# Performance work log

Hardware: AMD Instinct MI355X
Metric: run time of the kernel (lower is better)

## Reference

```python
import jax, jax.numpy as jnp
import numpy as np

NUM_HEAD = 16


def setup_inputs() -> dict:
    key = jax.random.key(0)
    ks = jax.random.split(key, 7)
    B, S, E = 2, 2048, 1024
    scale = 0.02
    return {
        "x": jax.random.normal(ks[0], (B, S, E), dtype=jnp.float32),
        "Wq": jax.random.normal(ks[1], (E, E), dtype=jnp.float32) * scale,
        "bq": jax.random.normal(ks[2], (E,), dtype=jnp.float32) * scale,
        "Wk": jax.random.normal(ks[3], (E, E), dtype=jnp.float32) * scale,
        "bk": jax.random.normal(ks[4], (E,), dtype=jnp.float32) * scale,
        "Wv": jax.random.normal(ks[5], (E, E), dtype=jnp.float32) * scale,
        "bv": jax.random.normal(ks[6], (E,), dtype=jnp.float32) * scale,
    }


def reference(x, Wq, bq, Wk, bk, Wv, bv):
    B, S, E = x.shape
    H = NUM_HEAD
    Dh = E // H
    # torch Linear: y = x @ W.T + b
    q = (x @ Wq.T + bq).reshape(B, S, H, Dh).transpose(0, 2, 1, 3)  # [B,H,S,Dh]
    k = (x @ Wk.T + bk).reshape(B, S, H, Dh).transpose(0, 2, 1, 3)
    v = (x @ Wv.T + bv).reshape(B, S, H, Dh).transpose(0, 2, 1, 3)
    attn = jnp.einsum("bhqd,bhkd->bhqk", q, k) / jnp.sqrt(jnp.float32(Dh))
    score = jax.nn.softmax(attn, axis=-1)
    out = jnp.einsum("bhqk,bhkd->bhqd", score, v)  # [B,H,S,Dh]
    return out.transpose(0, 2, 1, 3).reshape(B, S, E)
```

## Files before the change

### kernel.cpp

```cpp
#include <hip/hip_runtime.h>
#include <hip/hip_bf16.h>
#include <stdint.h>

#define S_LEN 2048
#define E_DIM 1024
#define NHEAD 16
#define DHEAD 64
#define BATCH 2

typedef short bf16x8 __attribute__((ext_vector_type(8)));
typedef float f32x4 __attribute__((ext_vector_type(4)));
typedef float f32x16 __attribute__((ext_vector_type(16)));

__device__ __forceinline__ ushort f2bf(float f) {
    uint32_t u = __builtin_bit_cast(uint32_t, f);
    u += 0x7fffu + ((u >> 16) & 1u);
    return (ushort)(u >> 16);
}
__device__ __forceinline__ uint32_t cvtpk(float lo, float hi) {
    uint32_t r;
    asm("v_cvt_pk_bf16_f32 %0, %1, %2" : "=v"(r) : "v"(lo), "v"(hi));
    return r;
}
__device__ __forceinline__ f32x16 zero16() {
    f32x16 v;
    #pragma unroll
    for (int i = 0; i < 16; ++i) v[i] = 0.f;
    return v;
}
__device__ __forceinline__ void gload16(const void* g, void* l) {
    __builtin_amdgcn_global_load_lds(
        (const __attribute__((address_space(1))) uint32_t*)g,
        (__attribute__((address_space(3))) uint32_t*)l, 16, 0, 0);
}

__global__ __launch_bounds__(256) void convert_kernel(
    const float* __restrict__ x, const float* __restrict__ wq,
    const float* __restrict__ wk, const float* __restrict__ wv,
    ushort* __restrict__ xb, ushort* __restrict__ wqb,
    ushort* __restrict__ wkb, ushort* __restrict__ wvb)
{
    const int a = blockIdx.y;
    const float* src = (a == 0) ? x : (a == 1) ? wq : (a == 2) ? wk : wv;
    ushort* dst      = (a == 0) ? xb : (a == 1) ? wqb : (a == 2) ? wkb : wvb;
    const int n4 = (a == 0) ? (BATCH * S_LEN * E_DIM / 4) : (E_DIM * E_DIM / 4);
    const int idx = blockIdx.x * 256 + threadIdx.x;
    if (idx < n4) {
        float4 v = reinterpret_cast<const float4*>(src)[idx];
        ushort4 o;
        o.x = f2bf(v.x); o.y = f2bf(v.y); o.z = f2bf(v.z); o.w = f2bf(v.w);
        reinterpret_cast<ushort4*>(dst)[idx] = o;
    }
}

__global__ __launch_bounds__(256) void qkv_mfma_kernel(
    const ushort* __restrict__ xb, const ushort* __restrict__ wqb,
    const ushort* __restrict__ wkb, const ushort* __restrict__ wvb,
    const float* __restrict__ bq, const float* __restrict__ bk,
    const float* __restrict__ bv,
    ushort* __restrict__ qb, ushort* __restrict__ kb, ushort* __restrict__ vtb)
{
    const int z = blockIdx.z;
    const ushort* Ag; const ushort* Bg; const float* bias;
    int m0, n0;
    if (z == 2) { Ag = wvb; Bg = xb;                 bias = bv;
                  m0 = blockIdx.y * 128; n0 = blockIdx.x * 128; }
    else        { Ag = xb;  Bg = (z == 0) ? wqb : wkb; bias = (z == 0) ? bq : bk;
                  m0 = blockIdx.x * 128; n0 = blockIdx.y * 128; }

    __shared__ ushort As[128 * 64];
    __shared__ ushort Bs[128 * 64];

    const int tid  = threadIdx.x;
    const int lane = tid & 63;
    const int wid  = tid >> 6;
    const int wr   = wid >> 1, wc = wid & 1;

    f32x4 acc[4][4];
    #pragma unroll
    for (int i = 0; i < 4; ++i)
        #pragma unroll
        for (int j = 0; j < 4; ++j) acc[i][j] = (f32x4){0.f, 0.f, 0.f, 0.f};

    const int crow  = lane >> 3;
    const int cslot = lane & 7;
    const int lr    = lane & 15;
    const int lq    = lane >> 4;

    for (int k0 = 0; k0 < E_DIM; k0 += 64) {
        #pragma unroll
        for (int j = 0; j < 4; ++j) {
            const int rbase = wid * 32 + j * 8;
            const int srow  = rbase + crow;
            const int sslot = cslot ^ (srow & 7);
            gload16(&Ag[(size_t)(m0 + srow) * E_DIM + k0 + sslot * 8],
                    &As[rbase * 64]);
            gload16(&Bg[(size_t)(n0 + srow) * E_DIM + k0 + sslot * 8],
                    &Bs[rbase * 64]);
        }
        __syncthreads();

        #pragma unroll
        for (int ks = 0; ks < 2; ++ks) {
            bf16x8 af[4], bf[4];
            #pragma unroll
            for (int mi = 0; mi < 4; ++mi) {
                const int row  = wr * 64 + mi * 16 + lr;
                const int slot = (ks * 4 + lq) ^ (row & 7);
                af[mi] = *reinterpret_cast<const bf16x8*>(
                    &As[row * 64 + slot * 8]);
            }
            #pragma unroll
            for (int ni = 0; ni < 4; ++ni) {
                const int row  = wc * 64 + ni * 16 + lr;
                const int slot = (ks * 4 + lq) ^ (row & 7);
                bf[ni] = *reinterpret_cast<const bf16x8*>(
                    &Bs[row * 64 + slot * 8]);
            }
            #pragma unroll
            for (int mi = 0; mi < 4; ++mi)
                #pragma unroll
                for (int ni = 0; ni < 4; ++ni)
                    acc[mi][ni] = __builtin_amdgcn_mfma_f32_16x16x32_bf16(
                        af[mi], bf[ni], acc[mi][ni], 0, 0, 0);
        }
        __syncthreads();
    }

    const int rq = lane >> 4;
    #pragma unroll
    for (int mi = 0; mi < 4; ++mi) {
        #pragma unroll
        for (int ni = 0; ni < 4; ++ni) {
            #pragma unroll
            for (int r = 0; r < 4; ++r) {
                const int i = m0 + wr * 64 + mi * 16 + rq * 4 + r;
                const int j = n0 + wc * 64 + ni * 16 + lr;
                float val = acc[mi][ni][r];
                if (z == 2) {
                    val += bias[i];
                    const int h = i >> 6, d = i & 63;
                    const int b = j >> 11, s = j & (S_LEN - 1);
                    vtb[(((size_t)(b * NHEAD + h)) * DHEAD + d) * S_LEN + s] = f2bf(val);
                } else {
                    val += bias[j];
                    const int h = j >> 6, d = j & 63;
                    const int b = i >> 11, s = i & (S_LEN - 1);
                    ushort* o = (z == 0) ? qb : kb;
                    o[(((size_t)(b * NHEAD + h)) * S_LEN + s) * DHEAD + d] = f2bf(val);
                }
            }
        }
    }
}

__global__ __launch_bounds__(512) void attn_mfma32_kernel(
    const ushort* __restrict__ qb, const ushort* __restrict__ kb,
    const ushort* __restrict__ vtb, float* __restrict__ out)
{
    const int bid = blockIdx.x;
    const int swzb = (bid & 7) * 32 + (bid >> 3);
    const int bh = swzb >> 3;
    const int q0 = (swzb & 7) * 256;
    const int b = bh >> 4, h = bh & 15;
    const ushort* Q  = qb  + (size_t)bh * S_LEN * DHEAD;
    const ushort* K  = kb  + (size_t)bh * S_LEN * DHEAD;
    const ushort* Vt = vtb + (size_t)bh * DHEAD * S_LEN;

    __shared__ ushort Qs[256 * 64];
    __shared__ ushort KV[2][2 * 64 * 64];

    const int tid  = threadIdx.x;
    const int lane = tid & 63;
    const int wid  = tid >> 6;
    const int hi   = lane >> 5;
    const int l31  = lane & 31;
    const int swzr = (lane & 7) << 3;
    const float SC = 0.125f;

    const int stslot = (tid & 7) * 8;
    const int strow  = tid >> 3;

    #pragma unroll
    for (int p = 0; p < 4; ++p) {
        const int row = strow + p * 64;
        bf16x8 v = *reinterpret_cast<const bf16x8*>(
            &Q[(size_t)(q0 + row) * DHEAD + stslot]);
        *reinterpret_cast<bf16x8*>(
            &Qs[row * 64 + (stslot ^ ((row & 7) << 3))]) = v;
    }

    bf16x8 kreg, vreg;
    kreg = *reinterpret_cast<const bf16x8*>(&K[(size_t)strow * DHEAD + stslot]);
    vreg = *reinterpret_cast<const bf16x8*>(&Vt[(size_t)strow * S_LEN + stslot]);
    __syncthreads();

    bf16x8 qf[4];
    {
        const int qrow = wid * 32 + l31;
        #pragma unroll
        for (int st = 0; st < 4; ++st)
            qf[st] = *reinterpret_cast<const bf16x8*>(
                &Qs[qrow * 64 + ((st * 16 + hi * 8) ^ ((qrow & 7) << 3))]);
    }

    {
        const int sw = strow * 64 + (stslot ^ ((strow & 7) << 3));
        *reinterpret_cast<bf16x8*>(&KV[0][sw])           = kreg;
        *reinterpret_cast<bf16x8*>(&KV[0][64 * 64 + sw]) = vreg;
    }
    __syncthreads();

    float m_run = -1e30f, l_run = 0.f;
    f32x16 oacc[2] = {zero16(), zero16()};
    int cur = 0;

    for (int t0 = 0; t0 < S_LEN; t0 += 64) {
        const bool more = (t0 + 64 < S_LEN);
        if (more) {
            const int tn = t0 + 64;
            kreg = *reinterpret_cast<const bf16x8*>(
                &K[(size_t)(tn + strow) * DHEAD + stslot]);
            vreg = *reinterpret_cast<const bf16x8*>(
                &Vt[(size_t)strow * S_LEN + tn + stslot]);
        }

        const ushort* Ks = &KV[cur][0];
        const ushort* Vs = &KV[cur][64 * 64];

        f32x16 sacc[2] = {zero16(), zero16()};
        #pragma unroll
        for (int t = 0; t < 2; ++t) {
            const int kbase = (t * 32 + l31) * 64;
            #pragma unroll
            for (int st = 0; st < 4; ++st) {
                bf16x8 kf = *reinterpret_cast<const bf16x8*>(
                    &Ks[kbase + ((st * 16 + hi * 8) ^ swzr)]);
                sacc[t] = __builtin_amdgcn_mfma_f32_32x32x16_bf16(
                    kf, qf[st], sacc[t], 0, 0, 0);
            }
        }

        float m8[8];
        #pragma unroll
        for (int i = 0; i < 8; ++i)
            m8[i] = fmaxf(fmaxf(sacc[0][i], sacc[0][i + 8]),
                          fmaxf(sacc[1][i], sacc[1][i + 8]));
        float mx = fmaxf(fmaxf(fmaxf(m8[0], m8[4]), fmaxf(m8[1], m8[5])),
                         fmaxf(fmaxf(m8[2], m8[6]), fmaxf(m8[3], m8[7])));
        mx = fmaxf(mx, __shfl_xor(mx, 32));
        const float mt = mx * SC;

        if (__any(mt > m_run + 8.0f)) {
            const float mn = fmaxf(m_run, mt);
            const float al = __expf(m_run - mn);
            m_run = mn;
            l_run *= al;
            #pragma unroll
            for (int r = 0; r < 16; ++r) { oacc[0][r] *= al; oacc[1][r] *= al; }
        }

        float csum[4];
        uint32_t w[4][4];
        #pragma unroll
        for (int t = 0; t < 2; ++t) {
            #pragma unroll
            for (int half = 0; half < 2; ++half) {
                float p[8];
                #pragma unroll
                for (int j = 0; j < 8; ++j)
                    p[j] = __expf(fmaf(sacc[t][half * 8 + j], SC, -m_run));
                const int c = t * 2 + half;
                csum[c] = (p[0] + p[1]) + (p[2] + p[3]) +
                          ((p[4] + p[5]) + (p[6] + p[7]));
                const uint32_t a0 = cvtpk(p[0], p[1]);
                const uint32_t a1 = cvtpk(p[2], p[3]);
                const uint32_t b0 = cvtpk(p[4], p[5]);
                const uint32_t b1 = cvtpk(p[6], p[7]);
                const uint32_t xs0 = __shfl_xor(a0, 32);
                const uint32_t ys0 = __shfl_xor(b0, 32);
                const uint32_t xs1 = __shfl_xor(a1, 32);
                const uint32_t ys1 = __shfl_xor(b1, 32);
                w[c][0] = hi ? ys0 : a0;
                w[c][2] = hi ? b0  : xs0;
                w[c][1] = hi ? ys1 : a1;
                w[c][3] = hi ? b1  : xs1;
            }
        }
        float lsum = (csum[0] + csum[1]) + (csum[2] + csum[3]);
        lsum += __shfl_xor(lsum, 32);
        l_run += lsum;

        #pragma unroll
        for (int c = 0; c < 4; ++c) {
            union { uint32_t u[4]; bf16x8 v; } pf;
            pf.u[0] = w[c][0]; pf.u[1] = w[c][1];
            pf.u[2] = w[c][2]; pf.u[3] = w[c][3];
            #pragma unroll
            for (int dblk = 0; dblk < 2; ++dblk) {
                const int vrow = dblk * 32 + l31;
                bf16x8 vf = *reinterpret_cast<const bf16x8*>(
                    &Vs[vrow * 64 + ((c * 16 + hi * 8) ^ swzr)]);
                oacc[dblk] = __builtin_amdgcn_mfma_f32_32x32x16_bf16(
                    vf, pf.v, oacc[dblk], 0, 0, 0);
            }
        }

        if (more) {
            __syncthreads();
            const int sw = strow * 64 + (stslot ^ ((strow & 7) << 3));
            *reinterpret_cast<bf16x8*>(&KV[cur ^ 1][sw])           = kreg;
            *reinterpret_cast<bf16x8*>(&KV[cur ^ 1][64 * 64 + sw]) = vreg;
            __syncthreads();
            cur ^= 1;
        }
    }

    const float inv = 1.f / l_run;
    const int qg = q0 + wid * 32 + l31;
    float* obase = &out[((size_t)(b * S_LEN + qg)) * E_DIM + h * DHEAD];
    #pragma unroll
    for (int dblk = 0; dblk < 2; ++dblk) {
        #pragma unroll
        for (int g = 0; g < 4; ++g) {
            float4 f;
            f.x = oacc[dblk][g * 4 + 0] * inv;
            f.y = oacc[dblk][g * 4 + 1] * inv;
            f.z = oacc[dblk][g * 4 + 2] * inv;
            f.w = oacc[dblk][g * 4 + 3] * inv;
            *reinterpret_cast<float4*>(&obase[dblk * 32 + g * 8 + hi * 4]) = f;
        }
    }
}

extern "C" void kernel_launch(void* const* d_in, const int* in_sizes, int n_in,
                              void* d_out, int out_size, void* d_ws, size_t ws_size,
                              hipStream_t stream) {
    const float* x  = (const float*)d_in[0];
    const float* Wq = (const float*)d_in[1];
    const float* bq = (const float*)d_in[2];
    const float* Wk = (const float*)d_in[3];
    const float* bk = (const float*)d_in[4];
    const float* Wv = (const float*)d_in[5];
    const float* bv = (const float*)d_in[6];
    float* out = (float*)d_out;

    const size_t XN = (size_t)BATCH * S_LEN * E_DIM;
    const size_t WN = (size_t)E_DIM * E_DIM;
    ushort* xb  = (ushort*)d_ws;
    ushort* wqb = xb  + XN;
    ushort* wkb = wqb + WN;
    ushort* wvb = wkb + WN;
    ushort* qbb = wvb + WN;
    ushort* kbb = qbb + XN;
    ushort* vtb = kbb + XN;

    convert_kernel<<<dim3(4096, 4), 256, 0, stream>>>(
        x, Wq, Wk, Wv, xb, wqb, wkb, wvb);

    qkv_mfma_kernel<<<dim3(32, 8, 3), 256, 0, stream>>>(
        xb, wqb, wkb, wvb, bq, bk, bv, qbb, kbb, vtb);

    attn_mfma32_kernel<<<dim3(256), 512, 0, stream>>>(qbb, kbb, vtb, out);
}
```

Baseline: 196.1 us.

## Double-buffer QKV GEMM tiles, use permlane32 swap and MFMA priority in attention

The QKV projection GEMM now uses two LDS buffers with a K-step of 32, so the next tile is loaded asynchronously while MFMAs run on the current one, and one barrier per step is removed. In the attention kernel, the four cross-half shuffles plus selects that repack P into bf16 operands are replaced by v_permlane32_swap instructions. The MFMA blocks are also wrapped in s_setprio to favour matrix issue across waves. The risks are the halved K-tile, which doubles loop iterations, and correctness of the swap semantics matching the old shuffle/select layout.

```diff
diff --git a/kernel.cpp b/kernel.cpp
--- a/kernel.cpp
+++ b/kernel.cpp
@@ -68,8 +68,8 @@
     else        { Ag = xb;  Bg = (z == 0) ? wqb : wkb; bias = (z == 0) ? bq : bk;
                   m0 = blockIdx.x * 128; n0 = blockIdx.y * 128; }
 
-    __shared__ ushort As[128 * 64];
-    __shared__ ushort Bs[128 * 64];
+    __shared__ ushort As[2][128 * 32];
+    __shared__ ushort Bs[2][128 * 32];
 
     const int tid  = threadIdx.x;
     const int lane = tid & 63;
@@ -82,48 +82,52 @@
         #pragma unroll
         for (int j = 0; j < 4; ++j) acc[i][j] = (f32x4){0.f, 0.f, 0.f, 0.f};
 
-    const int crow  = lane >> 3;
-    const int cslot = lane & 7;
+    const int crow  = lane >> 2;
+    const int cslot = lane & 3;
     const int lr    = lane & 15;
     const int lq    = lane >> 4;
 
-    for (int k0 = 0; k0 < E_DIM; k0 += 64) {
-        #pragma unroll
-        for (int j = 0; j < 4; ++j) {
-            const int rbase = wid * 32 + j * 8;
+    auto stage = [&](int bb, int k0) {
+        #pragma unroll
+        for (int j = 0; j < 2; ++j) {
+            const int rbase = wid * 32 + j * 16;
             const int srow  = rbase + crow;
-            const int sslot = cslot ^ (srow & 7);
-            gload16(&Ag[(size_t)(m0 + srow) * E_DIM + k0 + sslot * 8],
-                    &As[rbase * 64]);
-            gload16(&Bg[(size_t)(n0 + srow) * E_DIM + k0 + sslot * 8],
-                    &Bs[rbase * 64]);
-        }
-        __syncthreads();
-
-        #pragma unroll
-        for (int ks = 0; ks < 2; ++ks) {
-            bf16x8 af[4], bf[4];
-            #pragma unroll
-            for (int mi = 0; mi < 4; ++mi) {
-                const int row  = wr * 64 + mi * 16 + lr;
-                const int slot = (ks * 4 + lq) ^ (row & 7);
-                af[mi] = *reinterpret_cast<const bf16x8*>(
-                    &As[row * 64 + slot * 8]);
-            }
-            #pragma unroll
-            for (int ni = 0; ni < 4; ++ni) {
-                const int row  = wc * 64 + ni * 16 + lr;
-                const int slot = (ks * 4 + lq) ^ (row & 7);
-                bf[ni] = *reinterpret_cast<const bf16x8*>(
-                    &Bs[row * 64 + slot * 8]);
-            }
-            #pragma unroll
-            for (int mi = 0; mi < 4; ++mi)
-                #pragma unroll
-                for (int ni = 0; ni < 4; ++ni)
-                    acc[mi][ni] = __builtin_amdgcn_mfma_f32_16x16x32_bf16(
-                        af[mi], bf[ni], acc[mi][ni], 0, 0, 0);
-        }
+            const int ss    = cslot ^ (srow & 3);
+            gload16(&Ag[(size_t)(m0 + srow) * E_DIM + k0 + ss * 8],
+                    &As[bb][rbase * 32]);
+            gload16(&Bg[(size_t)(n0 + srow) * E_DIM + k0 + ss * 8],
+                    &Bs[bb][rbase * 32]);
+        }
+    };
+
+    stage(0, 0);
+    __syncthreads();
+
+    const int NT = E_DIM / 32;
+    for (int kt = 0; kt < NT; ++kt) {
+        const int bb = kt & 1;
+        if (kt + 1 < NT) stage(bb ^ 1, (kt + 1) * 32);
+
+        bf16x8 af[4], bf[4];
+        #pragma unroll
+        for (int mi = 0; mi < 4; ++mi) {
+            const int row = wr * 64 + mi * 16 + lr;
+            af[mi] = *reinterpret_cast<const bf16x8*>(
+                &As[bb][row * 32 + (lq ^ (row & 3)) * 8]);
+        }
+        #pragma unroll
+        for (int ni = 0; ni < 4; ++ni) {
+            const int row = wc * 64 + ni * 16 + lr;
+            bf[ni] = *reinterpret_cast<const bf16x8*>(
+                &Bs[bb][row * 32 + (lq ^ (row & 3)) * 8]);
+        }
+        #pragma unroll
+        for (int mi = 0; mi < 4; ++mi)
+            #pragma unroll
+            for (int ni = 0; ni < 4; ++ni)
+                acc[mi][ni] = __builtin_amdgcn_mfma_f32_16x16x32_bf16(
+                    af[mi], bf[ni], acc[mi][ni], 0, 0, 0);
+
         __syncthreads();
     }
 
@@ -229,6 +233,7 @@
         const ushort* Vs = &KV[cur][64 * 64];
 
         f32x16 sacc[2] = {zero16(), zero16()};
+        __builtin_amdgcn_s_setprio(1);
         #pragma unroll
         for (int t = 0; t < 2; ++t) {
             const int kbase = (t * 32 + l31) * 64;
@@ -240,6 +245,7 @@
                     kf, qf[st], sacc[t], 0, 0, 0);
             }
         }
+        __builtin_amdgcn_s_setprio(0);
 
         float m8[8];
         #pragma unroll
@@ -273,24 +279,22 @@
                 const int c = t * 2 + half;
                 csum[c] = (p[0] + p[1]) + (p[2] + p[3]) +
                           ((p[4] + p[5]) + (p[6] + p[7]));
-                const uint32_t a0 = cvtpk(p[0], p[1]);
-                const uint32_t a1 = cvtpk(p[2], p[3]);
-                const uint32_t b0 = cvtpk(p[4], p[5]);
-                const uint32_t b1 = cvtpk(p[6], p[7]);
-                const uint32_t xs0 = __shfl_xor(a0, 32);
-                const uint32_t ys0 = __shfl_xor(b0, 32);
-                const uint32_t xs1 = __shfl_xor(a1, 32);
-                const uint32_t ys1 = __shfl_xor(b1, 32);
-                w[c][0] = hi ? ys0 : a0;
-                w[c][2] = hi ? b0  : xs0;
-                w[c][1] = hi ? ys1 : a1;
-                w[c][3] = hi ? b1  : xs1;
+                uint32_t w0 = cvtpk(p[0], p[1]);
+                uint32_t w1 = cvtpk(p[2], p[3]);
+                uint32_t w2 = cvtpk(p[4], p[5]);
+                uint32_t w3 = cvtpk(p[6], p[7]);
+                asm volatile("v_permlane32_swap_b32 %0, %1"
+                             : "+v"(w0), "+v"(w2));
+                asm volatile("v_permlane32_swap_b32 %0, %1"
+                             : "+v"(w1), "+v"(w3));
+                w[c][0] = w0; w[c][1] = w1; w[c][2] = w2; w[c][3] = w3;
             }
         }
         float lsum = (csum[0] + csum[1]) + (csum[2] + csum[3]);
         lsum += __shfl_xor(lsum, 32);
         l_run += lsum;
 
+        __builtin_amdgcn_s_setprio(1);
         #pragma unroll
         for (int c = 0; c < 4; ++c) {
             union { uint32_t u[4]; bf16x8 v; } pf;
@@ -305,6 +309,7 @@
                     vf, pf.v, oacc[dblk], 0, 0, 0);
             }
         }
+        __builtin_amdgcn_s_setprio(0);
 
         if (more) {
             __syncthreads();
```

After: 184.7 us. 1.06x faster.
